# Kernel tuning notes

Measured on AMD Instinct MI355X. Metric: run time of the kernel, lower is better.

Reference implementation:

```python
import jax, jax.numpy as jnp
import numpy as np
import math

IN_C, OUT_C = 64, 128
OUT_C1 = int((OUT_C - IN_C) * 0.3 + IN_C)  # 83
OUT_C2 = int((OUT_C - IN_C) * 0.6 + IN_C)  # 102
OUT_C3 = OUT_C                              # 128
RESIDUE_RATIO = 0.5
R_RES = math.sqrt(RESIDUE_RATIO)
R_SC = math.sqrt(1.0 - RESIDUE_RATIO)
PRELU_INIT = 0.25
POST_MEAN = (1.0 - PRELU_INIT) / math.sqrt(2.0 * math.pi)
_POST_EX2 = (1.0 + PRELU_INIT ** 2) / 2.0
POST_STDV = math.sqrt(_POST_EX2 - POST_MEAN ** 2)


def _conv1x1_weight(key, out_c, in_c):
    # torch Conv1d custom init: normal_, then divide by per-out-channel L2 norm
    w = jax.random.normal(key, (out_c, in_c), dtype=jnp.float32)
    norm = jnp.sqrt(jnp.sum(w ** 2, axis=1, keepdims=True) + 1e-8)
    return w / norm


def cprelu(x, w):
    # x: [B, C, N], w: [C]
    y = jnp.where(x >= 0, x, x * w[None, :, None])
    return (y - POST_MEAN) / POST_STDV


def setup_inputs() -> dict:
    key = jax.random.key(0)
    ks = jax.random.split(key, 8)
    x = jax.random.normal(ks[0], (16, IN_C, 8192), dtype=jnp.float32)
    conn = jax.random.uniform(ks[1], (4096, 8192), dtype=jnp.float32)
    return {
        "x": x,
        "conn": conn,
        "w1": _conv1x1_weight(ks[2], OUT_C1, IN_C),
        "b1": jnp.zeros((OUT_C1,), jnp.float32),
        "p1": jnp.full((OUT_C1,), PRELU_INIT, jnp.float32),
        "w2": _conv1x1_weight(ks[3], OUT_C2, OUT_C1),
        "b2": jnp.zeros((OUT_C2,), jnp.float32),
        "p2": jnp.full((OUT_C2,), PRELU_INIT, jnp.float32),
        "wm": _conv1x1_weight(ks[4], OUT_C3, OUT_C2),
        "bm": jnp.zeros((OUT_C3,), jnp.float32),
        "p3": jnp.full((OUT_C3,), PRELU_INIT, jnp.float32),
        "ws": _conv1x1_weight(ks[5], OUT_C, IN_C),
        "bs": jnp.zeros((OUT_C,), jnp.float32),
    }


def _forward(x, conn, w1, b1, p1, w2, b2, p2, wm, bm, p3, ws, bs):
    # self-connection matrix: binary mask of per-row argmax entries (ties kept)
    sc = (conn - jnp.max(conn, axis=1, keepdims=True) >= 0).astype(jnp.float32)

    # residue branch: 1x1 conv -> CPReLU -> 1x1 conv -> CPReLU -> Meshconv -> CPReLU
    h = cprelu(jnp.einsum('bcn,oc->bon', x, w1) + b1[None, :, None], p1)
    h = cprelu(jnp.einsum('bcn,oc->bon', h, w2) + b2[None, :, None], p2)
    h = jnp.einsum('bcn,oc->bon', h, wm) + bm[None, :, None]      # [B, C3, Nin]
    h = jnp.einsum('oi,bci->bco', conn, h)                         # mesh pooling -> [B, C3, Nout]
    res = cprelu(h, p3)

    # shortcut branch: Meshconv with self_connection_matrix (1x1 conv + pooled gather)
    s = jnp.einsum('bcn,oc->bon', x, ws) + bs[None, :, None]       # [B, OUT_C, Nin]
    s = jnp.einsum('oi,bci->bco', sc, s)                           # [B, OUT_C, Nout]

    return s * R_SC + res * R_RES


def reference(x, conn, w1, b1, p1, w2, b2, p2, wm, bm, p3, ws, bs):
    return _forward(x, conn, w1, b1, p1, w2, b2, p2, wm, bm, p3, ws, bs)
```

## Files before the change

### kernel.cpp

```cpp
#include <hip/hip_runtime.h>
#include <hip/hip_bf16.h>
#include <stdint.h>

using bf16x8 = __attribute__((ext_vector_type(8))) __bf16;
using bf16x4 = __attribute__((ext_vector_type(4))) __bf16;
using f32x4  = __attribute__((ext_vector_type(4))) float;

typedef const uint32_t __attribute__((address_space(1)))* gas_ptr;
typedef uint32_t __attribute__((address_space(3)))* las_ptr;

__device__ __forceinline__ void load_lds16(const void* g, void* l) {
    __builtin_amdgcn_global_load_lds((gas_ptr)g, (las_ptr)l, 16, 0, 0);
}

#define PM  0.29920671030107454f
#define PIS 1.5046096f
#define RHALF 0.70710678118654752f

__global__ __launch_bounds__(256) void k_prep(const float* __restrict__ w1,
                                              const float* __restrict__ w2,
                                              const float* __restrict__ wm,
                                              const float* __restrict__ wsw,
                                              __bf16* __restrict__ W1p,
                                              __bf16* __restrict__ W2p,
                                              __bf16* __restrict__ WMp,
                                              __bf16* __restrict__ WSp)
{
    const int id = blockIdx.x * 256 + threadIdx.x;
    const int stride = gridDim.x * 256;
    for (int i = id; i < 96 * 64; i += stride) {
        int oc = i >> 6, ic = i & 63;
        W1p[i] = (__bf16)((oc < 83) ? w1[oc * 64 + ic] : 0.f);
    }
    for (int i = id; i < 112 * 96; i += stride) {
        int oc = i / 96, ic = i % 96;
        W2p[i] = (__bf16)((oc < 102 && ic < 83) ? w2[oc * 83 + ic] : 0.f);
    }
    for (int i = id; i < 128 * 128; i += stride) {
        int oc = i >> 7, ic = i & 127;
        WMp[i] = (__bf16)((ic < 102) ? wm[oc * 102 + ic] : 0.f);
    }
    for (int i = id; i < 128 * 64; i += stride) {
        WSp[i] = (__bf16)wsw[i];
    }
}

__global__ __launch_bounds__(256) void k_conv(const float* __restrict__ conn,
                                              __bf16* __restrict__ cb,
                                              size_t rowstride,
                                              int* __restrict__ cnt,
                                              int* __restrict__ idx)
{
    const int o = blockIdx.x;
    const int t = threadIdx.x;
    const float* row = conn + (size_t)o * 8192;
    float4 v[8];
    float m = -1e30f;
#pragma unroll
    for (int q = 0; q < 8; q++) {
        v[q] = *(const float4*)(row + (size_t)(q * 256 + t) * 4);
        m = fmaxf(m, fmaxf(fmaxf(v[q].x, v[q].y), fmaxf(v[q].z, v[q].w)));
    }
    __syncthreads();
    __bf16* drow = cb + (size_t)o * rowstride;
#pragma unroll
    for (int q = 0; q < 8; q++) {
        bf16x4 w;
        w[0] = (__bf16)v[q].x; w[1] = (__bf16)v[q].y;
        w[2] = (__bf16)v[q].z; w[3] = (__bf16)v[q].w;
        *(bf16x4*)(drow + (size_t)(q * 256 + t) * 4) = w;
    }
#pragma unroll
    for (int off = 32; off > 0; off >>= 1) m = fmaxf(m, __shfl_down(m, off, 64));
    __shared__ float wmax[4];
    __shared__ int scnt;
    if ((t & 63) == 0) wmax[t >> 6] = m;
    if (t == 0) scnt = 0;
    __syncthreads();
    const float rmax = fmaxf(fmaxf(wmax[0], wmax[1]), fmaxf(wmax[2], wmax[3]));
#pragma unroll
    for (int q = 0; q < 8; q++) {
        float vv[4] = {v[q].x, v[q].y, v[q].z, v[q].w};
#pragma unroll
        for (int e = 0; e < 4; e++) {
            if (vv[e] >= rmax) {
                int p = atomicAdd(&scnt, 1);
                if (p < 16) idx[o * 16 + p] = (q * 256 + t) * 4 + e;
            }
        }
    }
    __syncthreads();
    if (t == 0) cnt[o] = scnt < 16 ? scnt : 16;
}

template<int KS>
__device__ __forceinline__ f32x4 mfma_tile(const __bf16* __restrict__ W, int wstride, int mt,
                                           const __bf16* B, int bstride, int nt, int lane)
{
    f32x4 acc = {0.f, 0.f, 0.f, 0.f};
    const int l15 = lane & 15;
    const int kg  = (lane >> 4) << 3;
    const __bf16* wp = W + (mt * 16 + l15) * wstride + kg;
    const __bf16* bp = B + (nt * 16 + l15) * bstride + kg;
#pragma unroll
    for (int ks = 0; ks < KS; ks++) {
        bf16x8 av = *(const bf16x8*)(wp + ks * 32);
        bf16x8 bv = *(const bf16x8*)(bp + ks * 32);
        acc = __builtin_amdgcn_mfma_f32_16x16x32_bf16(av, bv, acc, 0, 0, 0);
    }
    return acc;
}

__global__ __launch_bounds__(256) void k_chain(
    const float* __restrict__ x,
    const float* __restrict__ b1, const float* __restrict__ p1,
    const float* __restrict__ b2, const float* __restrict__ p2,
    const float* __restrict__ bm, const float* __restrict__ bs,
    const __bf16* __restrict__ W1p, const __bf16* __restrict__ W2p,
    const __bf16* __restrict__ WMp, const __bf16* __restrict__ WSp,
    __bf16* __restrict__ h3, __bf16* __restrict__ s_t)
{
    __shared__ __bf16 buf0[64 * 136];
    __shared__ __bf16 un[128 * 72];
    __shared__ float  bl[672];
    __bf16* H1t  = un;
    __bf16* OutT = un;
    float* b1l = bl;       float* p1l = bl + 96;
    float* b2l = bl + 192; float* p2l = bl + 304;
    float* bml = bl + 416; float* bsl = bl + 544;

    const int t = threadIdx.x, lane = t & 63, wid = t >> 6;
    const int b = blockIdx.y;
    const int p0 = blockIdx.x * 64;

    for (int i = t; i < 96; i += 256)  { b1l[i] = (i < 83)  ? b1[i] : 0.f; p1l[i] = (i < 83)  ? p1[i] : 0.f; }
    for (int i = t; i < 112; i += 256) { b2l[i] = (i < 102) ? b2[i] : 0.f; p2l[i] = (i < 102) ? p2[i] : 0.f; }
    for (int i = t; i < 128; i += 256) { bml[i] = bm[i]; bsl[i] = bs[i]; }

    {
        const int p = t & 63;
        const int cg = t >> 6;
#pragma unroll 4
        for (int it = 0; it < 16; it++) {
            int c = it * 4 + cg;
            buf0[p * 72 + c] = (__bf16)x[((size_t)b * 64 + c) * 8192 + p0 + p];
        }
    }
    __syncthreads();

    const int quad4 = (lane >> 4) << 2;
    const int l15 = lane & 15;

    for (int tt = wid; tt < 32; tt += 4) {
        int mt = tt >> 2, nt = tt & 3;
        f32x4 a = mfma_tile<2>(WSp, 64, mt, buf0, 72, nt, lane);
        int ocb = mt * 16 + quad4;
        int pos = nt * 16 + l15;
        bf16x4 ov;
#pragma unroll
        for (int r = 0; r < 4; r++) ov[r] = (__bf16)(a[r] + bsl[ocb + r]);
        *(bf16x4*)(s_t + ((size_t)b * 8192 + p0 + pos) * 128 + ocb) = ov;
    }
    for (int tt = wid; tt < 24; tt += 4) {
        int mt = tt >> 2, nt = tt & 3;
        f32x4 a = mfma_tile<2>(W1p, 64, mt, buf0, 72, nt, lane);
        int ocb = mt * 16 + quad4;
        int pos = nt * 16 + l15;
        bf16x4 ov;
#pragma unroll
        for (int r = 0; r < 4; r++) {
            float v = a[r] + b1l[ocb + r];
            v = (v >= 0.f) ? v : v * p1l[ocb + r];
            ov[r] = (__bf16)((v - PM) * PIS);
        }
        *(bf16x4*)(&H1t[pos * 104 + ocb]) = ov;
    }
    __syncthreads();

    for (int tt = wid; tt < 28; tt += 4) {
        int mt = tt >> 2, nt = tt & 3;
        f32x4 a = mfma_tile<3>(W2p, 96, mt, H1t, 104, nt, lane);
        int ocb = mt * 16 + quad4;
        int pos = nt * 16 + l15;
        bf16x4 ov;
#pragma unroll
        for (int r = 0; r < 4; r++) {
            float v = a[r] + b2l[ocb + r];
            v = (v >= 0.f) ? v : v * p2l[ocb + r];
            ov[r] = (__bf16)((v - PM) * PIS);
        }
        *(bf16x4*)(&buf0[pos * 136 + ocb]) = ov;
    }
    for (int i = t; i < 64 * 16; i += 256) {
        int pos = i >> 4, c = 112 + (i & 15);
        buf0[pos * 136 + c] = (__bf16)0.f;
    }
    __syncthreads();

    for (int tt = wid; tt < 32; tt += 4) {
        int mt = tt >> 2, nt = tt & 3;
        f32x4 a = mfma_tile<4>(WMp, 128, mt, buf0, 136, nt, lane);
        int ocb = mt * 16 + quad4;
        int pos = nt * 16 + l15;
#pragma unroll
        for (int r = 0; r < 4; r++)
            OutT[(ocb + r) * 72 + pos] = (__bf16)(a[r] + bml[ocb + r]);
    }
    __syncthreads();

#pragma unroll
    for (int it = 0; it < 4; it++) {
        int lin = it * 256 + t;
        int ch = lin >> 3, pc = lin & 7;
        bf16x8 v = *(const bf16x8*)(OutT + ch * 72 + pc * 8);
        *(bf16x8*)(h3 + ((size_t)b * 128 + ch) * 8192 + p0 + pc * 8) = v;
    }
}

__global__ __launch_bounds__(256, 4) void k_gemm(const __bf16* __restrict__ A,
                                                 const __bf16* __restrict__ B,
                                                 size_t bstride,
                                                 float* __restrict__ C0,
                                                 float* __restrict__ C1,
                                                 int KH)
{
    __shared__ __bf16 la[128 * 64];
    __shared__ __bf16 lb[128 * 64];
    const int t = threadIdx.x;
    const int lane = t & 63;
    const int wid = t >> 6;
    const int tM = blockIdx.y * 128;
    const int tN = blockIdx.x * 128;
    const int kz = blockIdx.z;
    const int k0 = kz * KH;
    float* __restrict__ C = kz ? C1 : C0;
    const int wm2 = (wid & 1) * 64;
    const int wn2 = (wid >> 1) * 64;

    f32x4 acc[4][4];
    const f32x4 zero = {0.f, 0.f, 0.f, 0.f};
#pragma unroll
    for (int i = 0; i < 4; i++)
#pragma unroll
        for (int j = 0; j < 4; j++) acc[i][j] = zero;

    const int tr = t >> 3;
    const int sc = (t & 7) ^ (tr & 7);
    const __bf16* pA[4];
    const __bf16* pB[4];
#pragma unroll
    for (int i = 0; i < 4; i++) {
        pA[i] = A + (size_t)(tM + i * 32 + tr) * 8192 + k0 + sc * 8;
        pB[i] = B + (size_t)(tN + i * 32 + tr) * bstride + k0 + sc * 8;
    }

    const int l15 = lane & 15;
    const int q = lane >> 4;
    int aoff[4], boff[4];
#pragma unroll
    for (int i = 0; i < 4; i++) {
        int row = wm2 + i * 16 + l15;
        aoff[i] = row * 64 + ((q ^ (row & 7)) * 8);
    }
#pragma unroll
    for (int j = 0; j < 4; j++) {
        int row = wn2 + j * 16 + l15;
        boff[j] = row * 64 + ((q ^ (row & 7)) * 8);
    }

    const int iters = KH >> 6;
    for (int it = 0; it < iters; it++) {
#pragma unroll
        for (int i = 0; i < 4; i++) load_lds16(pA[i], la + (i * 256 + t) * 8);
#pragma unroll
        for (int i = 0; i < 4; i++) load_lds16(pB[i], lb + (i * 256 + t) * 8);
#pragma unroll
        for (int i = 0; i < 4; i++) { pA[i] += 64; pB[i] += 64; }
        __syncthreads();
#pragma unroll
        for (int ks = 0; ks < 2; ks++) {
            bf16x8 af[4], bfr[4];
#pragma unroll
            for (int i = 0; i < 4; i++) af[i]  = *(const bf16x8*)(la + (aoff[i] ^ (ks << 5)));
#pragma unroll
            for (int j = 0; j < 4; j++) bfr[j] = *(const bf16x8*)(lb + (boff[j] ^ (ks << 5)));
#pragma unroll
            for (int i = 0; i < 4; i++)
#pragma unroll
                for (int j = 0; j < 4; j++)
                    acc[i][j] = __builtin_amdgcn_mfma_f32_16x16x32_bf16(af[i], bfr[j], acc[i][j], 0, 0, 0);
        }
        __syncthreads();
    }

    const int quad4 = (lane >> 4) * 4;
#pragma unroll
    for (int i = 0; i < 4; i++) {
        int gm = tM + wm2 + i * 16 + quad4;
#pragma unroll
        for (int j = 0; j < 4; j++) {
            int gn = tN + wn2 + j * 16 + l15;
#pragma unroll
            for (int r = 0; r < 4; r++)
                C[(size_t)(gm + r) * 4096 + gn] = acc[i][j][r];
        }
    }
}

__global__ __launch_bounds__(256) void k_combine(float* __restrict__ out,
                                                 const float* __restrict__ P1,
                                                 int nsplit,
                                                 const __bf16* __restrict__ s_t,
                                                 const int* __restrict__ idx,
                                                 const int* __restrict__ cnt,
                                                 const float* __restrict__ p3)
{
    __shared__ float sp[64][133];
    const int b = blockIdx.y;
    const int o0 = blockIdx.x * 64;
    const int t = threadIdx.x;

    {
        const int ol = t >> 2;
        const int part = t & 3;
        const int o = o0 + ol;
        const int n = cnt[o];
        float acc[32];
#pragma unroll
        for (int j = 0; j < 32; j++) acc[j] = 0.f;
        for (int k = 0; k < n; k++) {
            const int i = idx[o * 16 + k];
            const __bf16* row = s_t + ((size_t)b * 8192 + i) * 128 + part * 32;
#pragma unroll
            for (int j = 0; j < 32; j += 8) {
                bf16x8 v = *(const bf16x8*)(row + j);
#pragma unroll
                for (int u = 0; u < 8; u++) acc[j + u] += (float)v[u];
            }
        }
#pragma unroll
        for (int j = 0; j < 32; j++) sp[ol][part * 32 + j] = acc[j];
    }
    __syncthreads();

    if (nsplit == 2) {
        for (int rr = 0; rr < 32; rr++) {
            const int c = rr * 4 + (t >> 6);
            const int o = t & 63;
            const size_t oi = ((size_t)b * 128 + c) * 4096 + o0 + o;
            float v = out[oi] + P1[oi];
            const float pw = p3[c];
            float y = (v >= 0.f) ? v : v * pw;
            y = (y - PM) * PIS;
            out[oi] = sp[o][c] * RHALF + y * RHALF;
        }
    } else {
        for (int rr = 0; rr < 32; rr++) {
            const int c = rr * 4 + (t >> 6);
            const int o = t & 63;
            const size_t oi = ((size_t)b * 128 + c) * 4096 + o0 + o;
            float v = out[oi];
            const float pw = p3[c];
            float y = (v >= 0.f) ? v : v * pw;
            y = (y - PM) * PIS;
            out[oi] = sp[o][c] * RHALF + y * RHALF;
        }
    }
}

extern "C" void kernel_launch(void* const* d_in, const int* in_sizes, int n_in,
                              void* d_out, int out_size, void* d_ws, size_t ws_size,
                              hipStream_t stream) {
    (void)in_sizes; (void)n_in; (void)out_size;
    const float* x    = (const float*)d_in[0];
    const float* conn = (const float*)d_in[1];
    const float* w1   = (const float*)d_in[2];
    const float* b1   = (const float*)d_in[3];
    const float* p1   = (const float*)d_in[4];
    const float* w2   = (const float*)d_in[5];
    const float* b2   = (const float*)d_in[6];
    const float* p2   = (const float*)d_in[7];
    const float* wm   = (const float*)d_in[8];
    const float* bm   = (const float*)d_in[9];
    const float* p3   = (const float*)d_in[10];
    const float* wsw  = (const float*)d_in[11];
    const float* bs   = (const float*)d_in[12];
    float* out = (float*)d_out;

    char* ws = (char*)d_ws;
    __bf16* h3  = (__bf16*)(ws);
    __bf16* s_t = (__bf16*)(ws + 33554432);
    __bf16* W1p = (__bf16*)(ws + 67108864);
    __bf16* W2p = (__bf16*)(ws + 67108864 + 12288);
    __bf16* WMp = (__bf16*)(ws + 67108864 + 33792);
    __bf16* WSp = (__bf16*)(ws + 67108864 + 66560);
    int* idx = (int*)(ws + 67108864 + 82944);
    int* cnt = (int*)(ws + 67108864 + 82944 + 262144);
    const size_t p1_off    = 67108864 + 82944 + 262144 + 16384;
    float* Pk1 = (float*)(ws + p1_off);
    const size_t connb_off = p1_off + 33554432;

    __bf16* connb;
    size_t  cstride;
    if (ws_size >= connb_off + (size_t)4096 * 8192 * 2) {
        connb = (__bf16*)(ws + connb_off);
        cstride = 8192;
    } else {
        connb = (__bf16*)const_cast<float*>(conn);
        cstride = 16384;
    }
    const int nsplit = (ws_size >= p1_off + 33554432) ? 2 : 1;
    const int KH = 8192 / nsplit;

    k_prep<<<32, 256, 0, stream>>>(w1, w2, wm, wsw, W1p, W2p, WMp, WSp);
    k_conv<<<4096, 256, 0, stream>>>(conn, connb, cstride, cnt, idx);
    k_chain<<<dim3(8192 / 64, 16), 256, 0, stream>>>(x, b1, p1, b2, p2, bm, bs,
                                                     W1p, W2p, WMp, WSp, h3, s_t);
    k_gemm<<<dim3(4096 / 128, 2048 / 128, nsplit), 256, 0, stream>>>(h3, connb, cstride,
                                                                     out, Pk1, KH);
    k_combine<<<dim3(4096 / 64, 16), 256, 0, stream>>>(out, Pk1, nsplit, s_t, idx, cnt, p3);
}
```

Before: 484.2 us.

## Rewrite mesh-pooling GEMM as 256x256 double-buffered, 8-wave pipelined MFMA kernel

Replaces the 128x128 single-buffered bf16 GEMM with 256x256 tiles computed by 512 threads (8 waves), using double-buffered LDS with global->LDS loads interleaved between MFMA clusters, s_setprio and sched barriers. It also remaps block indices for L2 locality. The intent is to hide global load latency behind MFMA work and raise arithmetic intensity per tile. The cost is much more LDS per block (128KB), fewer resident blocks, and a fragile waitcnt and barrier schedule.

```diff
diff --git a/kernel.cpp b/kernel.cpp
--- a/kernel.cpp
+++ b/kernel.cpp
@@ -217,94 +217,157 @@
     }
 }
 
-__global__ __launch_bounds__(256, 4) void k_gemm(const __bf16* __restrict__ A,
+#define GFENCE() asm volatile("" ::: "memory")
+#define GBAR()   do { GFENCE(); __builtin_amdgcn_s_barrier(); GFENCE(); } while (0)
+
+__global__ __launch_bounds__(512, 2) void k_gemm(const __bf16* __restrict__ A,
                                                  const __bf16* __restrict__ B,
                                                  size_t bstride,
                                                  float* __restrict__ C0,
                                                  float* __restrict__ C1,
                                                  int KH)
 {
-    __shared__ __bf16 la[128 * 64];
-    __shared__ __bf16 lb[128 * 64];
+    __shared__ __bf16 la[2][256 * 64];
+    __shared__ __bf16 lb[2][256 * 64];
+
     const int t = threadIdx.x;
     const int lane = t & 63;
     const int wid = t >> 6;
-    const int tM = blockIdx.y * 128;
-    const int tN = blockIdx.x * 128;
+    const int wm = wid >> 2;
+    const int wn = wid & 3;
+
+    const int orig = blockIdx.x;
+    const int swz  = (orig & 7) * 16 + (orig >> 3);
+    const int tN = (swz >> 3) * 256;
+    const int tM = (swz & 7) * 256;
     const int kz = blockIdx.z;
     const int k0 = kz * KH;
     float* __restrict__ C = kz ? C1 : C0;
-    const int wm2 = (wid & 1) * 64;
-    const int wn2 = (wid >> 1) * 64;
-
-    f32x4 acc[4][4];
-    const f32x4 zero = {0.f, 0.f, 0.f, 0.f};
-#pragma unroll
-    for (int i = 0; i < 4; i++)
-#pragma unroll
-        for (int j = 0; j < 4; j++) acc[i][j] = zero;
-
-    const int tr = t >> 3;
-    const int sc = (t & 7) ^ (tr & 7);
-    const __bf16* pA[4];
-    const __bf16* pB[4];
-#pragma unroll
-    for (int i = 0; i < 4; i++) {
-        pA[i] = A + (size_t)(tM + i * 32 + tr) * 8192 + k0 + sc * 8;
-        pB[i] = B + (size_t)(tN + i * 32 + tr) * bstride + k0 + sc * 8;
-    }
+
+    const int rA = t >> 3;
+    const int cA = (t & 7) ^ (rA & 7);
+    const __bf16* pA0 = A + (size_t)(tM + rA) * 8192 + k0 + cA * 8;
+    const __bf16* pA1 = pA0 + (size_t)128 * 8192;
+    const __bf16* pB0 = B + (size_t)(tN + rA) * bstride + k0 + cA * 8;
+    const __bf16* pB1 = pB0 + (size_t)128 * bstride;
+    const size_t iA = (size_t)64 * 8192;
+    const size_t iB = (size_t)64 * bstride;
+
+#define STG_A(d, h, kk) do { \
+    const __bf16* s_ = ((h) ? pA1 : pA0) + (kk); \
+    __bf16* l_ = &la[d][(h) * 8192 + t * 8]; \
+    load_lds16(s_, l_); \
+    load_lds16(s_ + iA, l_ + 4096); } while (0)
+#define STG_B(d, h, kk) do { \
+    const __bf16* s_ = ((h) ? pB1 : pB0) + (kk); \
+    __bf16* l_ = &lb[d][(h) * 8192 + t * 8]; \
+    load_lds16(s_, l_); \
+    load_lds16(s_ + iB, l_ + 4096); } while (0)
 
     const int l15 = lane & 15;
     const int q = lane >> 4;
-    int aoff[4], boff[4];
-#pragma unroll
-    for (int i = 0; i < 4; i++) {
-        int row = wm2 + i * 16 + l15;
-        aoff[i] = row * 64 + ((q ^ (row & 7)) * 8);
-    }
-#pragma unroll
-    for (int j = 0; j < 4; j++) {
-        int row = wn2 + j * 16 + l15;
-        boff[j] = row * 64 + ((q ^ (row & 7)) * 8);
-    }
-
-    const int iters = KH >> 6;
-    for (int it = 0; it < iters; it++) {
-#pragma unroll
-        for (int i = 0; i < 4; i++) load_lds16(pA[i], la + (i * 256 + t) * 8);
-#pragma unroll
-        for (int i = 0; i < 4; i++) load_lds16(pB[i], lb + (i * 256 + t) * 8);
-#pragma unroll
-        for (int i = 0; i < 4; i++) { pA[i] += 64; pB[i] += 64; }
-        __syncthreads();
-#pragma unroll
-        for (int ks = 0; ks < 2; ks++) {
-            bf16x8 af[4], bfr[4];
-#pragma unroll
-            for (int i = 0; i < 4; i++) af[i]  = *(const bf16x8*)(la + (aoff[i] ^ (ks << 5)));
-#pragma unroll
-            for (int j = 0; j < 4; j++) bfr[j] = *(const bf16x8*)(lb + (boff[j] ^ (ks << 5)));
-#pragma unroll
-            for (int i = 0; i < 4; i++)
-#pragma unroll
-                for (int j = 0; j < 4; j++)
-                    acc[i][j] = __builtin_amdgcn_mfma_f32_16x16x32_bf16(af[i], bfr[j], acc[i][j], 0, 0, 0);
-        }
-        __syncthreads();
-    }
-
-    const int quad4 = (lane >> 4) * 4;
-#pragma unroll
-    for (int i = 0; i < 4; i++) {
-        int gm = tM + wm2 + i * 16 + quad4;
-#pragma unroll
-        for (int j = 0; j < 4; j++) {
-            int gn = tN + wn2 + j * 16 + l15;
+    int aofs[2], bofs[2];
+#pragma unroll
+    for (int ks = 0; ks < 2; ks++) {
+        int sw = ((ks * 4 + q) ^ (l15 & 7)) * 8;
+        aofs[ks] = (wm * 128 + l15) * 64 + sw;
+        bofs[ks] = (wn * 64  + l15) * 64 + sw;
+    }
+#define LDA(d, m, ks) (*(const bf16x8*)(&la[d][aofs[ks] + (m) * 1024]))
+#define LDB(d, n, ks) (*(const bf16x8*)(&lb[d][bofs[ks] + (n) * 1024]))
+
+    f32x4 acc[8][4];
+    const f32x4 zero = {0.f, 0.f, 0.f, 0.f};
+#pragma unroll
+    for (int m = 0; m < 8; m++)
+#pragma unroll
+        for (int n = 0; n < 4; n++) acc[m][n] = zero;
+
+    bf16x8 af0[4][2], af1[4][2], bfr[4][2];
+
+#define CLUSTER(M0, N0, AF) do { \
+    __builtin_amdgcn_sched_barrier(0); \
+    __builtin_amdgcn_s_setprio(1); \
+    _Pragma("unroll") \
+    for (int ks_ = 0; ks_ < 2; ks_++) \
+        _Pragma("unroll") \
+        for (int m_ = 0; m_ < 4; m_++) \
+            _Pragma("unroll") \
+            for (int n_ = 0; n_ < 2; n_++) \
+                acc[(M0) + m_][(N0) + n_] = __builtin_amdgcn_mfma_f32_16x16x32_bf16( \
+                    AF[m_][ks_], bfr[(N0) + n_][ks_], acc[(M0) + m_][(N0) + n_], 0, 0, 0); \
+    __builtin_amdgcn_s_setprio(0); \
+    __builtin_amdgcn_sched_barrier(0); \
+} while (0)
+
+#define TILE_STEP(d, kkB, kkA) do { \
+     \
+    _Pragma("unroll") \
+    for (int m_ = 0; m_ < 4; m_++) { af0[m_][0] = LDA(d, m_, 0); af0[m_][1] = LDA(d, m_, 1); } \
+    _Pragma("unroll") \
+    for (int n_ = 0; n_ < 2; n_++) { bfr[n_][0] = LDB(d, n_, 0); bfr[n_][1] = LDB(d, n_, 1); } \
+    STG_B(1 - (d), 0, kkB); \
+    GBAR(); \
+    CLUSTER(0, 0, af0); \
+    GBAR(); \
+     \
+    _Pragma("unroll") \
+    for (int m_ = 0; m_ < 4; m_++) { af1[m_][0] = LDA(d, 4 + m_, 0); af1[m_][1] = LDA(d, 4 + m_, 1); } \
+    _Pragma("unroll") \
+    for (int n_ = 2; n_ < 4; n_++) { bfr[n_][0] = LDB(d, n_, 0); bfr[n_][1] = LDB(d, n_, 1); } \
+    STG_B(1 - (d), 1, kkB); \
+    GBAR(); \
+    CLUSTER(0, 2, af0); \
+    GBAR(); \
+     \
+    STG_A(d, 0, kkA); \
+    GBAR(); \
+    CLUSTER(4, 0, af1); \
+    GBAR(); \
+     \
+    STG_A(d, 1, kkA); \
+    GBAR(); \
+    CLUSTER(4, 2, af1); \
+    asm volatile("s_waitcnt vmcnt(4)" ::: "memory"); \
+    GBAR(); \
+} while (0)
+
+    STG_A(0, 0, 0); STG_A(0, 1, 0);
+    STG_B(0, 0, 0); STG_B(0, 1, 0);
+    STG_A(1, 0, 64); STG_A(1, 1, 64);
+    asm volatile("s_waitcnt vmcnt(4)" ::: "memory");
+    GBAR();
+
+    const int NT = KH >> 6;
+    for (int itp = 0; itp < (NT >> 1); ++itp) {
+        const int a = 2 * itp;
+        const int kkB_b = (a + 1) << 6;
+        int kkA_a2 = (a + 2) << 6; if (kkA_a2 >= KH) kkA_a2 -= KH;
+        int kkA_b2 = (a + 3) << 6; if (kkA_b2 >= KH) kkA_b2 -= KH;
+        TILE_STEP(0, kkB_b, kkA_a2);
+        TILE_STEP(1, kkA_a2, kkA_b2);
+    }
+
+    asm volatile("s_waitcnt vmcnt(0)" ::: "memory");
+
+    const int quad4 = q * 4;
+#pragma unroll
+    for (int m = 0; m < 8; m++) {
+        int gm = tM + wm * 128 + m * 16 + quad4;
+#pragma unroll
+        for (int n = 0; n < 4; n++) {
+            int gn = tN + wn * 64 + n * 16 + l15;
 #pragma unroll
             for (int r = 0; r < 4; r++)
-                C[(size_t)(gm + r) * 4096 + gn] = acc[i][j][r];
-        }
-    }
+                C[(size_t)(gm + r) * 4096 + gn] = acc[m][n][r];
+        }
+    }
+#undef TILE_STEP
+#undef CLUSTER
+#undef LDA
+#undef LDB
+#undef STG_A
+#undef STG_B
 }
 
 __global__ __launch_bounds__(256) void k_combine(float* __restrict__ out,
@@ -416,7 +479,6 @@
     k_conv<<<4096, 256, 0, stream>>>(conn, connb, cstride, cnt, idx);
     k_chain<<<dim3(8192 / 64, 16), 256, 0, stream>>>(x, b1, p1, b2, p2, bm, bs,
                                                      W1p, W2p, WMp, WSp, h3, s_t);
-    k_gemm<<<dim3(4096 / 128, 2048 / 128, nsplit), 256, 0, stream>>>(h3, connb, cstride,
-                                                                     out, Pk1, KH);
+    k_gemm<<<dim3(128, 1, nsplit), 512, 0, stream>>>(h3, connb, cstride, out, Pk1, KH);
     k_combine<<<dim3(4096 / 64, 16), 256, 0, stream>>>(out, Pk1, nsplit, s_t, idx, cnt, p3);
 }
```

After: 482.2 us. No clear change (-0.4%).

## Fuse conn conversion into chain kernel and combine epilogue into GEMM

Applied to the files above, without the earlier changes.

The conn bf16 conversion/argmax kernel and the 1x1-conv chain kernel are merged into one launch that interleaves two row-conversion blocks with one chain block per group. The GEMM drops its split-K (which wrote a second fp32 partial buffer) and instead runs the full K loop per tile. Its epilogue gathers the shortcut rows, applies CPReLU and the residual mix, and writes the output directly, removing the separate combine kernel. This saves launches and the partial-sum write/readback, but halves the GEMM grid parallelism and lowers occupancy (launch bounds 2, larger LDS).

```diff
diff --git a/kernel.cpp b/kernel.cpp
--- a/kernel.cpp
+++ b/kernel.cpp
@@ -45,54 +45,6 @@
     }
 }
 
-__global__ __launch_bounds__(256) void k_conv(const float* __restrict__ conn,
-                                              __bf16* __restrict__ cb,
-                                              size_t rowstride,
-                                              int* __restrict__ cnt,
-                                              int* __restrict__ idx)
-{
-    const int o = blockIdx.x;
-    const int t = threadIdx.x;
-    const float* row = conn + (size_t)o * 8192;
-    float4 v[8];
-    float m = -1e30f;
-#pragma unroll
-    for (int q = 0; q < 8; q++) {
-        v[q] = *(const float4*)(row + (size_t)(q * 256 + t) * 4);
-        m = fmaxf(m, fmaxf(fmaxf(v[q].x, v[q].y), fmaxf(v[q].z, v[q].w)));
-    }
-    __syncthreads();
-    __bf16* drow = cb + (size_t)o * rowstride;
-#pragma unroll
-    for (int q = 0; q < 8; q++) {
-        bf16x4 w;
-        w[0] = (__bf16)v[q].x; w[1] = (__bf16)v[q].y;
-        w[2] = (__bf16)v[q].z; w[3] = (__bf16)v[q].w;
-        *(bf16x4*)(drow + (size_t)(q * 256 + t) * 4) = w;
-    }
-#pragma unroll
-    for (int off = 32; off > 0; off >>= 1) m = fmaxf(m, __shfl_down(m, off, 64));
-    __shared__ float wmax[4];
-    __shared__ int scnt;
-    if ((t & 63) == 0) wmax[t >> 6] = m;
-    if (t == 0) scnt = 0;
-    __syncthreads();
-    const float rmax = fmaxf(fmaxf(wmax[0], wmax[1]), fmaxf(wmax[2], wmax[3]));
-#pragma unroll
-    for (int q = 0; q < 8; q++) {
-        float vv[4] = {v[q].x, v[q].y, v[q].z, v[q].w};
-#pragma unroll
-        for (int e = 0; e < 4; e++) {
-            if (vv[e] >= rmax) {
-                int p = atomicAdd(&scnt, 1);
-                if (p < 16) idx[o * 16 + p] = (q * 256 + t) * 4 + e;
-            }
-        }
-    }
-    __syncthreads();
-    if (t == 0) cnt[o] = scnt < 16 ? scnt : 16;
-}
-
 template<int KS>
 __device__ __forceinline__ f32x4 mfma_tile(const __bf16* __restrict__ W, int wstride, int mt,
                                            const __bf16* B, int bstride, int nt, int lane)
@@ -111,7 +63,9 @@
     return acc;
 }
 
-__global__ __launch_bounds__(256) void k_chain(
+__global__ __launch_bounds__(256) void k_cc(
+    const float* __restrict__ conn, __bf16* __restrict__ cb, size_t rowstride,
+    int* __restrict__ cnt, int* __restrict__ idx,
     const float* __restrict__ x,
     const float* __restrict__ b1, const float* __restrict__ p1,
     const float* __restrict__ b2, const float* __restrict__ p2,
@@ -120,18 +74,67 @@
     const __bf16* __restrict__ WMp, const __bf16* __restrict__ WSp,
     __bf16* __restrict__ h3, __bf16* __restrict__ s_t)
 {
-    __shared__ __bf16 buf0[64 * 136];
-    __shared__ __bf16 un[128 * 72];
-    __shared__ float  bl[672];
+    __shared__ __align__(16) char pool[38528];
+    const int t = threadIdx.x;
+    const int bx = blockIdx.x;
+    const int r3 = bx % 3;
+    const int g  = bx / 3;
+
+    if (r3 < 2) {
+        const int o = 2 * g + r3;
+        float* wmax = (float*)pool;
+        int*   scnt = (int*)(pool + 16);
+        const float* row = conn + (size_t)o * 8192;
+        float4 v[8];
+        float m = -1e30f;
+#pragma unroll
+        for (int q = 0; q < 8; q++) {
+            v[q] = *(const float4*)(row + (size_t)(q * 256 + t) * 4);
+            m = fmaxf(m, fmaxf(fmaxf(v[q].x, v[q].y), fmaxf(v[q].z, v[q].w)));
+        }
+        __syncthreads();
+        __bf16* drow = cb + (size_t)o * rowstride;
+#pragma unroll
+        for (int q = 0; q < 8; q++) {
+            bf16x4 w;
+            w[0] = (__bf16)v[q].x; w[1] = (__bf16)v[q].y;
+            w[2] = (__bf16)v[q].z; w[3] = (__bf16)v[q].w;
+            *(bf16x4*)(drow + (size_t)(q * 256 + t) * 4) = w;
+        }
+#pragma unroll
+        for (int off = 32; off > 0; off >>= 1) m = fmaxf(m, __shfl_down(m, off, 64));
+        if ((t & 63) == 0) wmax[t >> 6] = m;
+        if (t == 0) *scnt = 0;
+        __syncthreads();
+        const float rmax = fmaxf(fmaxf(wmax[0], wmax[1]), fmaxf(wmax[2], wmax[3]));
+#pragma unroll
+        for (int q = 0; q < 8; q++) {
+            float vv[4] = {v[q].x, v[q].y, v[q].z, v[q].w};
+#pragma unroll
+            for (int e = 0; e < 4; e++) {
+                if (vv[e] >= rmax) {
+                    int p = atomicAdd(scnt, 1);
+                    if (p < 16) idx[o * 16 + p] = (q * 256 + t) * 4 + e;
+                }
+            }
+        }
+        __syncthreads();
+        if (t == 0) cnt[o] = *scnt < 16 ? *scnt : 16;
+        return;
+    }
+
+    const int b  = g >> 7;
+    const int p0 = (g & 127) * 64;
+    __bf16* buf0 = (__bf16*)pool;
+    __bf16* un   = (__bf16*)(pool + 17408);
+    float*  bl   = (float*)(pool + 35840);
     __bf16* H1t  = un;
     __bf16* OutT = un;
     float* b1l = bl;       float* p1l = bl + 96;
     float* b2l = bl + 192; float* p2l = bl + 304;
     float* bml = bl + 416; float* bsl = bl + 544;
 
-    const int t = threadIdx.x, lane = t & 63, wid = t >> 6;
-    const int b = blockIdx.y;
-    const int p0 = blockIdx.x * 64;
+    const int lane = t & 63, wid = t >> 6;
 
     for (int i = t; i < 96; i += 256)  { b1l[i] = (i < 83)  ? b1[i] : 0.f; p1l[i] = (i < 83)  ? p1[i] : 0.f; }
     for (int i = t; i < 112; i += 256) { b2l[i] = (i < 102) ? b2[i] : 0.f; p2l[i] = (i < 102) ? p2[i] : 0.f; }
@@ -217,23 +220,26 @@
     }
 }
 
-__global__ __launch_bounds__(256, 4) void k_gemm(const __bf16* __restrict__ A,
+__global__ __launch_bounds__(256, 2) void k_gemm(const __bf16* __restrict__ A,
                                                  const __bf16* __restrict__ B,
                                                  size_t bstride,
-                                                 float* __restrict__ C0,
-                                                 float* __restrict__ C1,
-                                                 int KH)
+                                                 float* __restrict__ out,
+                                                 const __bf16* __restrict__ s_t,
+                                                 const int* __restrict__ idx,
+                                                 const int* __restrict__ cnt,
+                                                 const float* __restrict__ p3)
 {
-    __shared__ __bf16 la[128 * 64];
-    __shared__ __bf16 lb[128 * 64];
+    __shared__ __align__(16) char pool[66560];
+    __bf16* la = (__bf16*)pool;
+    __bf16* lb = (__bf16*)(pool + 16384);
+    float*  sp = (float*)pool;
+    float* p3l = (float*)(pool + 66048);
+
     const int t = threadIdx.x;
     const int lane = t & 63;
     const int wid = t >> 6;
     const int tM = blockIdx.y * 128;
     const int tN = blockIdx.x * 128;
-    const int kz = blockIdx.z;
-    const int k0 = kz * KH;
-    float* __restrict__ C = kz ? C1 : C0;
     const int wm2 = (wid & 1) * 64;
     const int wn2 = (wid >> 1) * 64;
 
@@ -250,8 +256,8 @@
     const __bf16* pB[4];
 #pragma unroll
     for (int i = 0; i < 4; i++) {
-        pA[i] = A + (size_t)(tM + i * 32 + tr) * 8192 + k0 + sc * 8;
-        pB[i] = B + (size_t)(tN + i * 32 + tr) * bstride + k0 + sc * 8;
+        pA[i] = A + (size_t)(tM + i * 32 + tr) * 8192 + sc * 8;
+        pB[i] = B + (size_t)(tN + i * 32 + tr) * bstride + sc * 8;
     }
 
     const int l15 = lane & 15;
@@ -268,8 +274,7 @@
         boff[j] = row * 64 + ((q ^ (row & 7)) * 8);
     }
 
-    const int iters = KH >> 6;
-    for (int it = 0; it < iters; it++) {
+    for (int it = 0; it < 128; it++) {
 #pragma unroll
         for (int i = 0; i < 4; i++) load_lds16(pA[i], la + (i * 256 + t) * 8);
 #pragma unroll
@@ -293,77 +298,52 @@
         __syncthreads();
     }
 
-    const int quad4 = (lane >> 4) * 4;
+    {
+        const int l = t >> 1;
+        const int part = t & 1;
+        const int col = tN + l;
+        const int n = cnt[col];
+        const __bf16* base = s_t + ((size_t)blockIdx.y * 8192) * 128 + part * 64;
+        float* spr = sp + l * 129 + part * 64;
+        {
+            const __bf16* row = base + (size_t)idx[col * 16] * 128;
+#pragma unroll
+            for (int j = 0; j < 8; j++) {
+                bf16x8 v = *(const bf16x8*)(row + j * 8);
+#pragma unroll
+                for (int u = 0; u < 8; u++) spr[j * 8 + u] = (float)v[u];
+            }
+        }
+        for (int k = 1; k < n; k++) {
+            const __bf16* row = base + (size_t)idx[col * 16 + k] * 128;
+#pragma unroll
+            for (int j = 0; j < 8; j++) {
+                bf16x8 v = *(const bf16x8*)(row + j * 8);
+#pragma unroll
+                for (int u = 0; u < 8; u++) spr[j * 8 + u] += (float)v[u];
+            }
+        }
+        if (t < 128) p3l[t] = p3[t];
+    }
+    __syncthreads();
+
+    const int quad4 = q * 4;
 #pragma unroll
     for (int i = 0; i < 4; i++) {
         int gm = tM + wm2 + i * 16 + quad4;
 #pragma unroll
         for (int j = 0; j < 4; j++) {
             int gn = tN + wn2 + j * 16 + l15;
-#pragma unroll
-            for (int r = 0; r < 4; r++)
-                C[(size_t)(gm + r) * 4096 + gn] = acc[i][j][r];
-        }
-    }
-}
-
-__global__ __launch_bounds__(256) void k_combine(float* __restrict__ out,
-                                                 const float* __restrict__ P1,
-                                                 int nsplit,
-                                                 const __bf16* __restrict__ s_t,
-                                                 const int* __restrict__ idx,
-                                                 const int* __restrict__ cnt,
-                                                 const float* __restrict__ p3)
-{
-    __shared__ float sp[64][133];
-    const int b = blockIdx.y;
-    const int o0 = blockIdx.x * 64;
-    const int t = threadIdx.x;
-
-    {
-        const int ol = t >> 2;
-        const int part = t & 3;
-        const int o = o0 + ol;
-        const int n = cnt[o];
-        float acc[32];
-#pragma unroll
-        for (int j = 0; j < 32; j++) acc[j] = 0.f;
-        for (int k = 0; k < n; k++) {
-            const int i = idx[o * 16 + k];
-            const __bf16* row = s_t + ((size_t)b * 8192 + i) * 128 + part * 32;
-#pragma unroll
-            for (int j = 0; j < 32; j += 8) {
-                bf16x8 v = *(const bf16x8*)(row + j);
-#pragma unroll
-                for (int u = 0; u < 8; u++) acc[j + u] += (float)v[u];
+            int colT = wn2 + j * 16 + l15;
+#pragma unroll
+            for (int r = 0; r < 4; r++) {
+                int c = wm2 + i * 16 + quad4 + r;
+                float v = acc[i][j][r];
+                float pw = p3l[c];
+                float y = (v >= 0.f) ? v : v * pw;
+                y = (y - PM) * PIS;
+                out[(size_t)(gm + r) * 4096 + gn] = sp[colT * 129 + c] * RHALF + y * RHALF;
             }
-        }
-#pragma unroll
-        for (int j = 0; j < 32; j++) sp[ol][part * 32 + j] = acc[j];
-    }
-    __syncthreads();
-
-    if (nsplit == 2) {
-        for (int rr = 0; rr < 32; rr++) {
-            const int c = rr * 4 + (t >> 6);
-            const int o = t & 63;
-            const size_t oi = ((size_t)b * 128 + c) * 4096 + o0 + o;
-            float v = out[oi] + P1[oi];
-            const float pw = p3[c];
-            float y = (v >= 0.f) ? v : v * pw;
-            y = (y - PM) * PIS;
-            out[oi] = sp[o][c] * RHALF + y * RHALF;
-        }
-    } else {
-        for (int rr = 0; rr < 32; rr++) {
-            const int c = rr * 4 + (t >> 6);
-            const int o = t & 63;
-            const size_t oi = ((size_t)b * 128 + c) * 4096 + o0 + o;
-            float v = out[oi];
-            const float pw = p3[c];
-            float y = (v >= 0.f) ? v : v * pw;
-            y = (y - PM) * PIS;
-            out[oi] = sp[o][c] * RHALF + y * RHALF;
         }
     }
 }
@@ -396,9 +376,7 @@
     __bf16* WSp = (__bf16*)(ws + 67108864 + 66560);
     int* idx = (int*)(ws + 67108864 + 82944);
     int* cnt = (int*)(ws + 67108864 + 82944 + 262144);
-    const size_t p1_off    = 67108864 + 82944 + 262144 + 16384;
-    float* Pk1 = (float*)(ws + p1_off);
-    const size_t connb_off = p1_off + 33554432;
+    const size_t connb_off = 67108864 + 82944 + 262144 + 16384;
 
     __bf16* connb;
     size_t  cstride;
@@ -409,14 +387,11 @@
         connb = (__bf16*)const_cast<float*>(conn);
         cstride = 16384;
     }
-    const int nsplit = (ws_size >= p1_off + 33554432) ? 2 : 1;
-    const int KH = 8192 / nsplit;
 
     k_prep<<<32, 256, 0, stream>>>(w1, w2, wm, wsw, W1p, W2p, WMp, WSp);
-    k_conv<<<4096, 256, 0, stream>>>(conn, connb, cstride, cnt, idx);
-    k_chain<<<dim3(8192 / 64, 16), 256, 0, stream>>>(x, b1, p1, b2, p2, bm, bs,
-                                                     W1p, W2p, WMp, WSp, h3, s_t);
-    k_gemm<<<dim3(4096 / 128, 2048 / 128, nsplit), 256, 0, stream>>>(h3, connb, cstride,
-                                                                     out, Pk1, KH);
-    k_combine<<<dim3(4096 / 64, 16), 256, 0, stream>>>(out, Pk1, nsplit, s_t, idx, cnt, p3);
-}
+    k_cc<<<6144, 256, 0, stream>>>(conn, connb, cstride, cnt, idx,
+                                   x, b1, p1, b2, p2, bm, bs,
+                                   W1p, W2p, WMp, WSp, h3, s_t);
+    k_gemm<<<dim3(4096 / 128, 2048 / 128), 256, 0, stream>>>(h3, connb, cstride,
+                                                             out, s_t, idx, cnt, p3);
+}
```

Measured after the change: 467.1 us. -3.5%, faster.

## Fuse combine epilogue into GEMM, drop split-K, use 128x64 tiles with swizzled order

Applied to the files above, without the earlier changes.

The separate combine kernel is removed. Its gather-sum of the shortcut rows, the CPReLU on the mesh-pool result and the residual mix now run in the GEMM epilogue, straight from registers. Split-K and its fp32 partial buffer go away, and the GEMM switches to 128x64 tiles over a full K of 8192 with a remapped block order meant to improve L2 reuse. This removes the round trips of the output and partial buffers through global memory. The cost is a longer serial K loop per block and scattered gather loads in the epilogue.

```diff
diff --git a/kernel.cpp b/kernel.cpp
--- a/kernel.cpp
+++ b/kernel.cpp
@@ -220,150 +220,128 @@
 __global__ __launch_bounds__(256, 4) void k_gemm(const __bf16* __restrict__ A,
                                                  const __bf16* __restrict__ B,
                                                  size_t bstride,
-                                                 float* __restrict__ C0,
-                                                 float* __restrict__ C1,
-                                                 int KH)
-{
-    __shared__ __bf16 la[128 * 64];
-    __shared__ __bf16 lb[128 * 64];
-    const int t = threadIdx.x;
-    const int lane = t & 63;
-    const int wid = t >> 6;
-    const int tM = blockIdx.y * 128;
-    const int tN = blockIdx.x * 128;
-    const int kz = blockIdx.z;
-    const int k0 = kz * KH;
-    float* __restrict__ C = kz ? C1 : C0;
-    const int wm2 = (wid & 1) * 64;
-    const int wn2 = (wid >> 1) * 64;
-
-    f32x4 acc[4][4];
-    const f32x4 zero = {0.f, 0.f, 0.f, 0.f};
-#pragma unroll
-    for (int i = 0; i < 4; i++)
-#pragma unroll
-        for (int j = 0; j < 4; j++) acc[i][j] = zero;
-
-    const int tr = t >> 3;
-    const int sc = (t & 7) ^ (tr & 7);
-    const __bf16* pA[4];
-    const __bf16* pB[4];
-#pragma unroll
-    for (int i = 0; i < 4; i++) {
-        pA[i] = A + (size_t)(tM + i * 32 + tr) * 8192 + k0 + sc * 8;
-        pB[i] = B + (size_t)(tN + i * 32 + tr) * bstride + k0 + sc * 8;
-    }
-
-    const int l15 = lane & 15;
-    const int q = lane >> 4;
-    int aoff[4], boff[4];
-#pragma unroll
-    for (int i = 0; i < 4; i++) {
-        int row = wm2 + i * 16 + l15;
-        aoff[i] = row * 64 + ((q ^ (row & 7)) * 8);
-    }
-#pragma unroll
-    for (int j = 0; j < 4; j++) {
-        int row = wn2 + j * 16 + l15;
-        boff[j] = row * 64 + ((q ^ (row & 7)) * 8);
-    }
-
-    const int iters = KH >> 6;
-    for (int it = 0; it < iters; it++) {
-#pragma unroll
-        for (int i = 0; i < 4; i++) load_lds16(pA[i], la + (i * 256 + t) * 8);
-#pragma unroll
-        for (int i = 0; i < 4; i++) load_lds16(pB[i], lb + (i * 256 + t) * 8);
-#pragma unroll
-        for (int i = 0; i < 4; i++) { pA[i] += 64; pB[i] += 64; }
-        __syncthreads();
-#pragma unroll
-        for (int ks = 0; ks < 2; ks++) {
-            bf16x8 af[4], bfr[4];
-#pragma unroll
-            for (int i = 0; i < 4; i++) af[i]  = *(const bf16x8*)(la + (aoff[i] ^ (ks << 5)));
-#pragma unroll
-            for (int j = 0; j < 4; j++) bfr[j] = *(const bf16x8*)(lb + (boff[j] ^ (ks << 5)));
-#pragma unroll
-            for (int i = 0; i < 4; i++)
-#pragma unroll
-                for (int j = 0; j < 4; j++)
-                    acc[i][j] = __builtin_amdgcn_mfma_f32_16x16x32_bf16(af[i], bfr[j], acc[i][j], 0, 0, 0);
-        }
-        __syncthreads();
-    }
-
-    const int quad4 = (lane >> 4) * 4;
-#pragma unroll
-    for (int i = 0; i < 4; i++) {
-        int gm = tM + wm2 + i * 16 + quad4;
-#pragma unroll
-        for (int j = 0; j < 4; j++) {
-            int gn = tN + wn2 + j * 16 + l15;
-#pragma unroll
-            for (int r = 0; r < 4; r++)
-                C[(size_t)(gm + r) * 4096 + gn] = acc[i][j][r];
-        }
-    }
-}
-
-__global__ __launch_bounds__(256) void k_combine(float* __restrict__ out,
-                                                 const float* __restrict__ P1,
-                                                 int nsplit,
+                                                 float* __restrict__ out,
                                                  const __bf16* __restrict__ s_t,
                                                  const int* __restrict__ idx,
                                                  const int* __restrict__ cnt,
                                                  const float* __restrict__ p3)
 {
-    __shared__ float sp[64][133];
-    const int b = blockIdx.y;
-    const int o0 = blockIdx.x * 64;
+    __shared__ __bf16 la[128 * 64];
+    __shared__ __bf16 lb[64 * 64];
+
     const int t = threadIdx.x;
-
-    {
-        const int ol = t >> 2;
-        const int part = t & 3;
-        const int o = o0 + ol;
-        const int n = cnt[o];
-        float acc[32];
-#pragma unroll
-        for (int j = 0; j < 32; j++) acc[j] = 0.f;
+    const int lane = t & 63;
+    const int wid = t >> 6;
+
+    const int hw  = blockIdx.y * 64 + blockIdx.x;
+    const int nid = (hw & 7) * 128 + (hw >> 3);
+    const int tMi = nid >> 6;
+    const int tM  = tMi * 128;
+    const int tN  = (nid & 63) * 64;
+
+    const int wm2 = (wid & 1) * 64;
+    const int wn2 = (wid >> 1) * 32;
+
+    f32x4 acc[4][2];
+    const f32x4 zero = {0.f, 0.f, 0.f, 0.f};
+#pragma unroll
+    for (int i = 0; i < 4; i++)
+#pragma unroll
+        for (int j = 0; j < 2; j++) acc[i][j] = zero;
+
+    const int tr = t >> 3;
+    const int sc = (t & 7) ^ (tr & 7);
+    const __bf16* pA[4];
+    const __bf16* pB[2];
+#pragma unroll
+    for (int i = 0; i < 4; i++)
+        pA[i] = A + (size_t)(tM + i * 32 + tr) * 8192 + sc * 8;
+#pragma unroll
+    for (int i = 0; i < 2; i++)
+        pB[i] = B + (size_t)(tN + i * 32 + tr) * bstride + sc * 8;
+
+    const int l15 = lane & 15;
+    const int q = lane >> 4;
+    int aoff[4], boff[2];
+#pragma unroll
+    for (int i = 0; i < 4; i++) {
+        int row = wm2 + i * 16 + l15;
+        aoff[i] = row * 64 + ((q ^ (row & 7)) * 8);
+    }
+#pragma unroll
+    for (int j = 0; j < 2; j++) {
+        int row = wn2 + j * 16 + l15;
+        boff[j] = row * 64 + ((q ^ (row & 7)) * 8);
+    }
+
+    for (int it = 0; it < 128; it++) {
+#pragma unroll
+        for (int i = 0; i < 4; i++) load_lds16(pA[i], la + (i * 256 + t) * 8);
+#pragma unroll
+        for (int i = 0; i < 2; i++) load_lds16(pB[i], lb + (i * 256 + t) * 8);
+#pragma unroll
+        for (int i = 0; i < 4; i++) pA[i] += 64;
+#pragma unroll
+        for (int i = 0; i < 2; i++) pB[i] += 64;
+        __syncthreads();
+#pragma unroll
+        for (int ks = 0; ks < 2; ks++) {
+            bf16x8 af[4], bfr[2];
+#pragma unroll
+            for (int i = 0; i < 4; i++) af[i]  = *(const bf16x8*)(la + (aoff[i] ^ (ks << 5)));
+#pragma unroll
+            for (int j = 0; j < 2; j++) bfr[j] = *(const bf16x8*)(lb + (boff[j] ^ (ks << 5)));
+#pragma unroll
+            for (int i = 0; i < 4; i++)
+#pragma unroll
+                for (int j = 0; j < 2; j++)
+                    acc[i][j] = __builtin_amdgcn_mfma_f32_16x16x32_bf16(af[i], bfr[j], acc[i][j], 0, 0, 0);
+        }
+        __syncthreads();
+    }
+
+    const int quad4 = q * 4;
+
+    f32x4 pw[4];
+#pragma unroll
+    for (int i = 0; i < 4; i++)
+        pw[i] = *(const f32x4*)(p3 + wm2 + i * 16 + quad4);
+
+    f32x4 spv[2][4];
+#pragma unroll
+    for (int j = 0; j < 2; j++)
+#pragma unroll
+        for (int i = 0; i < 4; i++) spv[j][i] = zero;
+
+    const __bf16* sbase = s_t + ((size_t)tMi * 8192) * 128;
+#pragma unroll
+    for (int j = 0; j < 2; j++) {
+        const int col = tN + wn2 + j * 16 + l15;
+        const int n = cnt[col];
         for (int k = 0; k < n; k++) {
-            const int i = idx[o * 16 + k];
-            const __bf16* row = s_t + ((size_t)b * 8192 + i) * 128 + part * 32;
-#pragma unroll
-            for (int j = 0; j < 32; j += 8) {
-                bf16x8 v = *(const bf16x8*)(row + j);
-#pragma unroll
-                for (int u = 0; u < 8; u++) acc[j + u] += (float)v[u];
+            const __bf16* row = sbase + (size_t)idx[col * 16 + k] * 128;
+#pragma unroll
+            for (int i = 0; i < 4; i++) {
+                bf16x4 v = *(const bf16x4*)(row + wm2 + i * 16 + quad4);
+#pragma unroll
+                for (int r = 0; r < 4; r++) spv[j][i][r] += (float)v[r];
             }
         }
-#pragma unroll
-        for (int j = 0; j < 32; j++) sp[ol][part * 32 + j] = acc[j];
-    }
-    __syncthreads();
-
-    if (nsplit == 2) {
-        for (int rr = 0; rr < 32; rr++) {
-            const int c = rr * 4 + (t >> 6);
-            const int o = t & 63;
-            const size_t oi = ((size_t)b * 128 + c) * 4096 + o0 + o;
-            float v = out[oi] + P1[oi];
-            const float pw = p3[c];
-            float y = (v >= 0.f) ? v : v * pw;
-            y = (y - PM) * PIS;
-            out[oi] = sp[o][c] * RHALF + y * RHALF;
-        }
-    } else {
-        for (int rr = 0; rr < 32; rr++) {
-            const int c = rr * 4 + (t >> 6);
-            const int o = t & 63;
-            const size_t oi = ((size_t)b * 128 + c) * 4096 + o0 + o;
-            float v = out[oi];
-            const float pw = p3[c];
-            float y = (v >= 0.f) ? v : v * pw;
-            y = (y - PM) * PIS;
-            out[oi] = sp[o][c] * RHALF + y * RHALF;
+    }
+
+#pragma unroll
+    for (int i = 0; i < 4; i++) {
+        const int gm = tM + wm2 + i * 16 + quad4;
+#pragma unroll
+        for (int j = 0; j < 2; j++) {
+            const int gn = tN + wn2 + j * 16 + l15;
+#pragma unroll
+            for (int r = 0; r < 4; r++) {
+                float v = acc[i][j][r];
+                float y = (v >= 0.f) ? v : v * pw[i][r];
+                y = (y - PM) * PIS;
+                out[(size_t)(gm + r) * 4096 + gn] = spv[j][i][r] * RHALF + y * RHALF;
+            }
         }
     }
 }
@@ -396,9 +374,7 @@
     __bf16* WSp = (__bf16*)(ws + 67108864 + 66560);
     int* idx = (int*)(ws + 67108864 + 82944);
     int* cnt = (int*)(ws + 67108864 + 82944 + 262144);
-    const size_t p1_off    = 67108864 + 82944 + 262144 + 16384;
-    float* Pk1 = (float*)(ws + p1_off);
-    const size_t connb_off = p1_off + 33554432;
+    const size_t connb_off = 67108864 + 82944 + 262144 + 16384;
 
     __bf16* connb;
     size_t  cstride;
@@ -409,14 +385,10 @@
         connb = (__bf16*)const_cast<float*>(conn);
         cstride = 16384;
     }
-    const int nsplit = (ws_size >= p1_off + 33554432) ? 2 : 1;
-    const int KH = 8192 / nsplit;
 
     k_prep<<<32, 256, 0, stream>>>(w1, w2, wm, wsw, W1p, W2p, WMp, WSp);
     k_conv<<<4096, 256, 0, stream>>>(conn, connb, cstride, cnt, idx);
     k_chain<<<dim3(8192 / 64, 16), 256, 0, stream>>>(x, b1, p1, b2, p2, bm, bs,
                                                      W1p, W2p, WMp, WSp, h3, s_t);
-    k_gemm<<<dim3(4096 / 128, 2048 / 128, nsplit), 256, 0, stream>>>(h3, connb, cstride,
-                                                                     out, Pk1, KH);
-    k_combine<<<dim3(4096 / 64, 16), 256, 0, stream>>>(out, Pk1, nsplit, s_t, idx, cnt, p3);
-}
+    k_gemm<<<dim3(64, 16), 256, 0, stream>>>(h3, connb, cstride, out, s_t, idx, cnt, p3);
+}
```

After: 513.1 us. +6.0%, slower.
